# Kernel optimization log

Measured on AMD Instinct MI355X. Metric: run time of the kernel, lower is better.

Reference implementation:

```python
import jax, jax.numpy as jnp
import numpy as np

N = 50000   # nodes
E = 800000  # edges
IN, HID, OUT = 128, 128, 64


def setup_inputs() -> dict:
    key = jax.random.key(0)
    ks = jax.random.split(key, 16)
    x = jax.random.normal(ks[0], (N, IN), dtype=jnp.float32)
    src = jax.random.randint(ks[1], (E,), 0, N, dtype=jnp.int32)
    dst = jax.random.randint(ks[2], (E,), 0, N, dtype=jnp.int32)
    s = 1.0 / np.sqrt(IN)
    W_self1 = jax.random.normal(ks[3], (IN, HID), dtype=jnp.float32) * s
    W_neigh1 = jax.random.normal(ks[4], (IN, HID), dtype=jnp.float32) * s
    b1 = jnp.zeros((HID,), dtype=jnp.float32)
    W_self2 = jax.random.normal(ks[5], (HID, HID), dtype=jnp.float32) * s
    W_neigh2 = jax.random.normal(ks[6], (HID, HID), dtype=jnp.float32) * s
    b2 = jnp.zeros((HID,), dtype=jnp.float32)
    W_self3 = jax.random.normal(ks[7], (HID, OUT), dtype=jnp.float32) * s
    W_neigh3 = jax.random.normal(ks[8], (HID, OUT), dtype=jnp.float32) * s
    b3 = jnp.zeros((OUT,), dtype=jnp.float32)
    # dropout(p=0.5) masks, pre-scaled by 1/(1-p)
    keep = 0.5
    mask1 = (jax.random.uniform(ks[9], (N, HID)) < keep).astype(jnp.float32) / keep
    mask2 = (jax.random.uniform(ks[10], (N, HID)) < keep).astype(jnp.float32) / keep
    return dict(x=x, src=src, dst=dst,
                W_self1=W_self1, W_neigh1=W_neigh1, b1=b1,
                W_self2=W_self2, W_neigh2=W_neigh2, b2=b2,
                W_self3=W_self3, W_neigh3=W_neigh3, b3=b3,
                mask1=mask1, mask2=mask2)


def _mean_agg(h, src, dst):
    # gather source features, segment-sum into destinations, divide by in-degree
    summed = jax.ops.segment_sum(h[src], dst, num_segments=N)  # [N, d]
    deg = jax.ops.segment_sum(jnp.ones((E,), dtype=h.dtype), dst, num_segments=N)
    return summed / jnp.maximum(deg, 1.0)[:, None]


def _sage_layer(h, src, dst, W_self, W_neigh, b):
    h_neigh = _mean_agg(h, src, dst)
    return h @ W_self + h_neigh @ W_neigh + b


def reference(x, src, dst, W_self1, W_neigh1, b1, W_self2, W_neigh2, b2,
              W_self3, W_neigh3, b3, mask1, mask2):
    h = _sage_layer(x, src, dst, W_self1, W_neigh1, b1)
    h = jax.nn.relu(h) * mask1
    h = _sage_layer(h, src, dst, W_self2, W_neigh2, b2)
    h = jax.nn.relu(h) * mask2
    h = _sage_layer(h, src, dst, W_self3, W_neigh3, b3)
    return h
```

## Files before the change

### kernel.cpp

```cpp
#include <hip/hip_runtime.h>
#include <hip/hip_bf16.h>

#define DIN  128
#define DHID 128
#define DOUT 64

typedef short short8 __attribute__((ext_vector_type(8)));
typedef float f32x4  __attribute__((ext_vector_type(4)));

__device__ __forceinline__ ushort f2bf(float f) {
    union { float f; uint u; } c; c.f = f;
    uint u = c.u;
    return (ushort)((u + 0x7fff + ((u >> 16) & 1)) >> 16);
}
__device__ __forceinline__ float bf2f(uint h16) {
    union { uint u; float f; } c; c.u = h16 << 16;
    return c.f;
}
__device__ __forceinline__ float sb8(uint u, int k) {
    return (float)((int)(u << (24 - 8 * k)) >> 24);
}

__device__ __forceinline__ void wprep_dev(const float* __restrict__ W,
                                          ushort* __restrict__ Wt, int OUT, int idx) {
    int nn = idx >> 7;
    int k  = idx & 127;
    Wt[idx] = f2bf(W[(size_t)k * OUT + nn]);
}

__global__ __launch_bounds__(256)
void prep_all(const float* __restrict__ x, ushort* __restrict__ xb, int n4, int cvtB,
              const float* __restrict__ Ws1, const float* __restrict__ Wn1,
              const float* __restrict__ Ws2, const float* __restrict__ Wn2,
              const float* __restrict__ Ws3, const float* __restrict__ Wn3,
              ushort* __restrict__ Wst1, ushort* __restrict__ Wnt1,
              ushort* __restrict__ Wst2, ushort* __restrict__ Wnt2,
              ushort* __restrict__ Wst3, ushort* __restrict__ Wnt3) {
    int b = blockIdx.x;
    if (b < cvtB) {
        int i = b * 256 + threadIdx.x;
        if (i < n4) {
            float4 v = ((const float4*)x)[i];
            ushort4 o;
            o.x = f2bf(v.x); o.y = f2bf(v.y); o.z = f2bf(v.z); o.w = f2bf(v.w);
            ((ushort4*)xb)[i] = o;
        }
        return;
    }
    b -= cvtB;
    if (b < 64)  { wprep_dev(Ws1, Wst1, 128, b * 256 + threadIdx.x); return; }
    b -= 64;
    if (b < 64)  { wprep_dev(Wn1, Wnt1, 128, b * 256 + threadIdx.x); return; }
    b -= 64;
    if (b < 64)  { wprep_dev(Ws2, Wst2, 128, b * 256 + threadIdx.x); return; }
    b -= 64;
    if (b < 64)  { wprep_dev(Wn2, Wnt2, 128, b * 256 + threadIdx.x); return; }
    b -= 64;
    if (b < 32)  { wprep_dev(Ws3, Wst3, 64, b * 256 + threadIdx.x); return; }
    b -= 32;
    wprep_dev(Wn3, Wnt3, 64, b * 256 + threadIdx.x);
}

#define EB 4096

__global__ __launch_bounds__(256)
void bucket_count(const int* __restrict__ dst, int E, int* __restrict__ bkt_cnt) {
    __shared__ int c[256];
    const int t = threadIdx.x;
    c[t] = 0;
    __syncthreads();
    const int base = blockIdx.x * EB;
    const int end = min(base + EB, E);
    for (int i = base + t; i < end; i += 256)
        atomicAdd(&c[dst[i] >> 8], 1);
    __syncthreads();
    int v = c[t];
    if (v) atomicAdd(&bkt_cnt[t], v);
}

__global__ __launch_bounds__(256)
void bucket_scan(const int* __restrict__ bkt_cnt, int nbkt,
                 int* __restrict__ bkt_base, int* __restrict__ bkt_cur) {
    __shared__ int s[256];
    const int t = threadIdx.x;
    int v = (t < nbkt) ? bkt_cnt[t] : 0;
    s[t] = v;
    __syncthreads();
    for (int o = 1; o < 256; o <<= 1) {
        int u = (t >= o) ? s[t - o] : 0;
        __syncthreads();
        s[t] += u;
        __syncthreads();
    }
    if (t < nbkt) { bkt_base[t] = s[t] - v; bkt_cur[t] = s[t] - v; }
}

__global__ __launch_bounds__(256)
void bucket_fill(const int* __restrict__ src, const int* __restrict__ dst, int E,
                 int* __restrict__ bkt_cur, uint2* __restrict__ pairs) {
    __shared__ int c[256];
    __shared__ int startl[256];
    __shared__ int ofs[256];
    const int t = threadIdx.x;
    c[t] = 0;
    __syncthreads();
    const int base = blockIdx.x * EB;
    const int end = min(base + EB, E);
    for (int i = base + t; i < end; i += 256)
        atomicAdd(&c[dst[i] >> 8], 1);
    __syncthreads();
    int v = c[t];
    startl[t] = v ? atomicAdd(&bkt_cur[t], v) : 0;
    ofs[t] = 0;
    __syncthreads();
    for (int i = base + t; i < end; i += 256) {
        int d = dst[i];
        int b = d >> 8;
        int p = startl[b] + atomicAdd(&ofs[b], 1);
        pairs[p] = make_uint2((uint)src[i], (uint)(d & 255));
    }
}

__global__ __launch_bounds__(256)
void bucket_csr(const uint2* __restrict__ pairs, const int* __restrict__ bkt_base,
                const int* __restrict__ bkt_cnt, int* __restrict__ row_ptr,
                int* __restrict__ esrc, int N, int E, int nbkt) {
    constexpr int CAP = 6144;
    __shared__ uint2 pl[CAP];
    __shared__ int cnt[256];
    __shared__ int rs[256];
    __shared__ int sc[256];
    const int bkt = blockIdx.x;
    const int t = threadIdx.x;
    const int ebase = bkt_base[bkt];
    const int ecnt  = bkt_cnt[bkt];
    cnt[t] = 0;
    __syncthreads();
    const bool fits = (ecnt <= CAP);
    if (fits) {
        for (int i = t; i < ecnt; i += 256) {
            uint2 p = pairs[ebase + i];
            pl[i] = p;
            atomicAdd(&cnt[p.y], 1);
        }
    } else {
        for (int i = t; i < ecnt; i += 256)
            atomicAdd(&cnt[pairs[ebase + i].y], 1);
    }
    __syncthreads();
    int own = cnt[t];
    sc[t] = own;
    __syncthreads();
    for (int o = 1; o < 256; o <<= 1) {
        int u = (t >= o) ? sc[t - o] : 0;
        __syncthreads();
        sc[t] += u;
        __syncthreads();
    }
    rs[t] = sc[t] - own;
    const int node = bkt * 256 + t;
    if (node < N) row_ptr[node] = ebase + rs[t];
    if (bkt == nbkt - 1 && t == 0) row_ptr[N] = E;
    __syncthreads();
    if (fits) {
        for (int i = t; i < ecnt; i += 256) {
            uint2 p = pl[i];
            int pos = atomicAdd(&rs[p.y], 1);
            esrc[ebase + pos] = (int)p.x;
        }
    } else {
        for (int i = t; i < ecnt; i += 256) {
            uint2 p = pairs[ebase + i];
            int pos = atomicAdd(&rs[p.y], 1);
            esrc[ebase + pos] = (int)p.x;
        }
    }
}

template<int OUTW>
__global__ __launch_bounds__(256)
void sage_gemm(const ushort* __restrict__ Hb,
               const ushort* __restrict__ Wst,
               const ushort* __restrict__ Wnt,
               ushort* __restrict__ S,
               signed char* __restrict__ Gq,
               float* __restrict__ Gsc,
               int n) {
    constexpr int NT = OUTW / 16;
    __shared__ ushort Wl[2][OUTW * 128];

    const int tid  = threadIdx.x;
    const int lane = tid & 63;
    const int wave = tid >> 6;
    const int rg   = wave >> 1;
    const int isG  = wave & 1;
    const int m16  = lane & 15;
    const int kb   = lane >> 4;
    const int rbase = blockIdx.x * 64 + rg * 32;

    {
        const uint4* s4 = (const uint4*)Wst;
        const uint4* n4 = (const uint4*)Wnt;
        uint4* ls = (uint4*)&Wl[0][0];
        uint4* ln = (uint4*)&Wl[1][0];
#pragma unroll
        for (int j = tid; j < OUTW * 128 / 8; j += 256) {
            ls[j] = s4[j];
            ln[j] = n4[j];
        }
    }

    short8 a[2][4];
#pragma unroll
    for (int mt = 0; mt < 2; ++mt) {
        int arow = rbase + mt * 16 + m16;
        if (arow >= n) arow = n - 1;
        const ushort* __restrict__ Ap = &Hb[(size_t)arow * 128 + kb * 8];
#pragma unroll
        for (int c = 0; c < 4; ++c)
            a[mt][c] = *(const short8*)(Ap + c * 32);
    }

    __syncthreads();

    f32x4 acc[2][NT];
#pragma unroll
    for (int mt = 0; mt < 2; ++mt)
#pragma unroll
        for (int t = 0; t < NT; ++t) acc[mt][t] = (f32x4)(0.f);

    const ushort* __restrict__ Wp = &Wl[isG][0];
#pragma unroll
    for (int t = 0; t < NT; ++t) {
#pragma unroll
        for (int c = 0; c < 4; ++c) {
            short8 b = *(const short8*)&Wp[(t * 16 + m16) * 128 + c * 32 + kb * 8];
            acc[0][t] = __builtin_amdgcn_mfma_f32_16x16x32_bf16(a[0][c], b, acc[0][t], 0, 0, 0);
            acc[1][t] = __builtin_amdgcn_mfma_f32_16x16x32_bf16(a[1][c], b, acc[1][t], 0, 0, 0);
        }
    }

#pragma unroll
    for (int mt = 0; mt < 2; ++mt) {
        const int rb = rbase + mt * 16;
        if (!isG) {
#pragma unroll
            for (int r = 0; r < 4; ++r) {
                int row = rb + kb * 4 + r;
                if (row >= n) continue;
#pragma unroll
                for (int t = 0; t < NT; ++t)
                    S[(size_t)row * OUTW + t * 16 + m16] = f2bf(acc[mt][t][r]);
            }
        } else {
#pragma unroll
            for (int r = 0; r < 4; ++r) {
                float mx = 0.f;
#pragma unroll
                for (int t = 0; t < NT; ++t) mx = fmaxf(mx, fabsf(acc[mt][t][r]));
                mx = fmaxf(mx, __shfl_xor(mx, 1));
                mx = fmaxf(mx, __shfl_xor(mx, 2));
                mx = fmaxf(mx, __shfl_xor(mx, 4));
                mx = fmaxf(mx, __shfl_xor(mx, 8));
                int row = rb + kb * 4 + r;
                if (row >= n) continue;
                float inv = (mx > 0.f) ? 127.f / mx : 0.f;
                if (m16 == 0) Gsc[row] = mx * (1.f / 127.f);
#pragma unroll
                for (int t = 0; t < NT; ++t) {
                    int q = (int)rintf(acc[mt][t][r] * inv);
                    q = max(-127, min(127, q));
                    Gq[(size_t)row * OUTW + t * 16 + m16] = (signed char)q;
                }
            }
        }
    }
}

__device__ __forceinline__ void acc8(float* af, uint2 v, float sc) {
    af[0] += sc * sb8(v.x, 0); af[1] += sc * sb8(v.x, 1);
    af[2] += sc * sb8(v.x, 2); af[3] += sc * sb8(v.x, 3);
    af[4] += sc * sb8(v.y, 0); af[5] += sc * sb8(v.y, 1);
    af[6] += sc * sb8(v.y, 2); af[7] += sc * sb8(v.y, 3);
}
__device__ __forceinline__ void acc4(float* af, uint v, float sc) {
    af[0] += sc * sb8(v, 0); af[1] += sc * sb8(v, 1);
    af[2] += sc * sb8(v, 2); af[3] += sc * sb8(v, 3);
}

template<int OUTW, bool FINAL>
__global__ __launch_bounds__(256)
void sage_gather(const signed char* __restrict__ Gq, const float* __restrict__ Gsc,
                 const ushort* __restrict__ S, const float* __restrict__ bias,
                 const float* __restrict__ mask,
                 const int* __restrict__ row_ptr, const int* __restrict__ esrc,
                 void* __restrict__ outv, int n) {
    const int lane = threadIdx.x & 63;
    const int wave = threadIdx.x >> 6;
    const int qw   = lane >> 4;
    const int l16  = lane & 15;

#pragma unroll
    for (int j = 0; j < 2; ++j) {
        const int node = blockIdx.x * 32 + (wave * 4 + qw) * 2 + j;
        if (node >= n) continue;
        const int s = row_ptr[node];
        const int e = row_ptr[node + 1];
        const float inv = 1.f / fmaxf((float)(e - s), 1.f);

        if (OUTW == 128) {
            const signed char* __restrict__ gp = Gq + l16 * 8;
            float af[8] = {0.f, 0.f, 0.f, 0.f, 0.f, 0.f, 0.f, 0.f};
            int i = s;
            for (; i + 3 < e; i += 4) {
                int n0 = esrc[i], n1 = esrc[i + 1], n2 = esrc[i + 2], n3 = esrc[i + 3];
                uint2 v0 = *(const uint2*)&gp[(size_t)n0 * 128];
                uint2 v1 = *(const uint2*)&gp[(size_t)n1 * 128];
                uint2 v2 = *(const uint2*)&gp[(size_t)n2 * 128];
                uint2 v3 = *(const uint2*)&gp[(size_t)n3 * 128];
                float c0 = Gsc[n0], c1 = Gsc[n1], c2 = Gsc[n2], c3 = Gsc[n3];
                acc8(af, v0, c0); acc8(af, v1, c1); acc8(af, v2, c2); acc8(af, v3, c3);
            }
            for (; i < e; ++i) {
                int ns = esrc[i];
                uint2 v = *(const uint2*)&gp[(size_t)ns * 128];
                acc8(af, v, Gsc[ns]);
            }
            const int col0 = l16 * 8;
            uint4 sv = *(const uint4*)&S[(size_t)node * 128 + col0];
            float4 b0 = *(const float4*)&bias[col0];
            float4 b1 = *(const float4*)&bias[col0 + 4];
            float z[8];
            z[0] = bf2f(sv.x & 0xffffu) + af[0] * inv + b0.x;
            z[1] = bf2f(sv.x >> 16)     + af[1] * inv + b0.y;
            z[2] = bf2f(sv.y & 0xffffu) + af[2] * inv + b0.z;
            z[3] = bf2f(sv.y >> 16)     + af[3] * inv + b0.w;
            z[4] = bf2f(sv.z & 0xffffu) + af[4] * inv + b1.x;
            z[5] = bf2f(sv.z >> 16)     + af[5] * inv + b1.y;
            z[6] = bf2f(sv.w & 0xffffu) + af[6] * inv + b1.z;
            z[7] = bf2f(sv.w >> 16)     + af[7] * inv + b1.w;
            float4 m0 = *(const float4*)&mask[(size_t)node * 128 + col0];
            float4 m1 = *(const float4*)&mask[(size_t)node * 128 + col0 + 4];
            z[0] = fmaxf(z[0], 0.f) * m0.x; z[1] = fmaxf(z[1], 0.f) * m0.y;
            z[2] = fmaxf(z[2], 0.f) * m0.z; z[3] = fmaxf(z[3], 0.f) * m0.w;
            z[4] = fmaxf(z[4], 0.f) * m1.x; z[5] = fmaxf(z[5], 0.f) * m1.y;
            z[6] = fmaxf(z[6], 0.f) * m1.z; z[7] = fmaxf(z[7], 0.f) * m1.w;
            uint4 pk;
            pk.x = (uint)f2bf(z[0]) | ((uint)f2bf(z[1]) << 16);
            pk.y = (uint)f2bf(z[2]) | ((uint)f2bf(z[3]) << 16);
            pk.z = (uint)f2bf(z[4]) | ((uint)f2bf(z[5]) << 16);
            pk.w = (uint)f2bf(z[6]) | ((uint)f2bf(z[7]) << 16);
            *(uint4*)&((ushort*)outv)[(size_t)node * 128 + col0] = pk;
        } else {
            const signed char* __restrict__ gp = Gq + l16 * 4;
            float af[4] = {0.f, 0.f, 0.f, 0.f};
            int i = s;
            for (; i + 3 < e; i += 4) {
                int n0 = esrc[i], n1 = esrc[i + 1], n2 = esrc[i + 2], n3 = esrc[i + 3];
                uint v0 = *(const uint*)&gp[(size_t)n0 * 64];
                uint v1 = *(const uint*)&gp[(size_t)n1 * 64];
                uint v2 = *(const uint*)&gp[(size_t)n2 * 64];
                uint v3 = *(const uint*)&gp[(size_t)n3 * 64];
                float c0 = Gsc[n0], c1 = Gsc[n1], c2 = Gsc[n2], c3 = Gsc[n3];
                acc4(af, v0, c0); acc4(af, v1, c1); acc4(af, v2, c2); acc4(af, v3, c3);
            }
            for (; i < e; ++i) {
                int ns = esrc[i];
                uint v = *(const uint*)&gp[(size_t)ns * 64];
                acc4(af, v, Gsc[ns]);
            }
            const int col0 = l16 * 4;
            uint2 sv = *(const uint2*)&S[(size_t)node * 64 + col0];
            float4 b0 = *(const float4*)&bias[col0];
            float4 z;
            z.x = bf2f(sv.x & 0xffffu) + af[0] * inv + b0.x;
            z.y = bf2f(sv.x >> 16)     + af[1] * inv + b0.y;
            z.z = bf2f(sv.y & 0xffffu) + af[2] * inv + b0.z;
            z.w = bf2f(sv.y >> 16)     + af[3] * inv + b0.w;
            *(float4*)&((float*)outv)[(size_t)node * 64 + col0] = z;
        }
    }
}

extern "C" void kernel_launch(void* const* d_in, const int* in_sizes, int n_in,
                              void* d_out, int out_size, void* d_ws, size_t ws_size,
                              hipStream_t stream) {
    const float* x   = (const float*)d_in[0];
    const int*   src = (const int*)d_in[1];
    const int*   dst = (const int*)d_in[2];
    const float* Ws1 = (const float*)d_in[3];
    const float* Wn1 = (const float*)d_in[4];
    const float* b1  = (const float*)d_in[5];
    const float* Ws2 = (const float*)d_in[6];
    const float* Wn2 = (const float*)d_in[7];
    const float* b2  = (const float*)d_in[8];
    const float* Ws3 = (const float*)d_in[9];
    const float* Wn3 = (const float*)d_in[10];
    const float* b3  = (const float*)d_in[11];
    const float* mask1 = (const float*)d_in[12];
    const float* mask2 = (const float*)d_in[13];
    float* out = (float*)d_out;

    const int N = in_sizes[0] / DIN;
    const int E = in_sizes[1];
    const int nbkt = (N + 255) >> 8;

    char* ws = (char*)d_ws;
    int* bkt_cnt  = (int*)ws;
    int* bkt_base = bkt_cnt + 256;
    int* bkt_cur  = bkt_base + 256;
    int* row_ptr  = bkt_cur + 256;
    int* esrc     = row_ptr + (N + 1);
    size_t off = ((size_t)(768 + N + 1 + E) * sizeof(int) + 255) & ~(size_t)255;
    uint2* pairs = (uint2*)(ws + off);   off += (size_t)E * 8;
    ushort* xb   = (ushort*)(ws + off);  off += (size_t)N * 128 * 2;
    ushort* h1b  = (ushort*)(ws + off);  off += (size_t)N * 128 * 2;
    ushort* h2b  = (ushort*)(ws + off);  off += (size_t)N * 128 * 2;
    ushort* S    = (ushort*)(ws + off);  off += (size_t)N * 128 * 2;
    signed char* Gq = (signed char*)(ws + off); off += (size_t)N * 128;
    float* Gsc   = (float*)(ws + off);   off += (size_t)N * 4;
    ushort* Wst1 = (ushort*)(ws + off);  off += 128 * 128 * 2;
    ushort* Wnt1 = (ushort*)(ws + off);  off += 128 * 128 * 2;
    ushort* Wst2 = (ushort*)(ws + off);  off += 128 * 128 * 2;
    ushort* Wnt2 = (ushort*)(ws + off);  off += 128 * 128 * 2;
    ushort* Wst3 = (ushort*)(ws + off);  off += 64 * 128 * 2;
    ushort* Wnt3 = (ushort*)(ws + off);  off += 64 * 128 * 2;

    const int n4 = N * 128 / 4;
    const int cvtB = (n4 + 255) / 256;
    const int ebB = (E + EB - 1) / EB;

    hipMemsetAsync(bkt_cnt, 0, 256 * sizeof(int), stream);
    prep_all<<<cvtB + 4 * 64 + 2 * 32, 256, 0, stream>>>(
        x, xb, n4, cvtB,
        Ws1, Wn1, Ws2, Wn2, Ws3, Wn3,
        Wst1, Wnt1, Wst2, Wnt2, Wst3, Wnt3);

    bucket_count<<<ebB, 256, 0, stream>>>(dst, E, bkt_cnt);
    bucket_scan<<<1, 256, 0, stream>>>(bkt_cnt, nbkt, bkt_base, bkt_cur);
    bucket_fill<<<ebB, 256, 0, stream>>>(src, dst, E, bkt_cur, pairs);
    bucket_csr<<<nbkt, 256, 0, stream>>>(pairs, bkt_base, bkt_cnt, row_ptr, esrc, N, E, nbkt);

    const int gemmB = (N + 63) / 64;
    const int gathB = (N + 31) / 32;

    sage_gemm<128><<<gemmB, 256, 0, stream>>>(xb, Wst1, Wnt1, S, Gq, Gsc, N);
    sage_gather<128, false><<<gathB, 256, 0, stream>>>(Gq, Gsc, S, b1, mask1, row_ptr, esrc, h1b, N);
    sage_gemm<128><<<gemmB, 256, 0, stream>>>(h1b, Wst2, Wnt2, S, Gq, Gsc, N);
    sage_gather<128, false><<<gathB, 256, 0, stream>>>(Gq, Gsc, S, b2, mask2, row_ptr, esrc, h2b, N);
    sage_gemm<64><<<gemmB, 256, 0, stream>>>(h2b, Wst3, Wnt3, S, Gq, Gsc, N);
    sage_gather<64, true><<<gathB, 256, 0, stream>>>(Gq, Gsc, S, b3, nullptr, row_ptr, esrc, out, N);
}
```

Before: 304.4 us.

## Fuse bucket count into prep kernel and split CSR rows by source half

Folds the destination-bucket counting pass into the prep_all kernel, removing one launch. The CSR build now sorts each row's edges into two segments by whether the source index falls below or above N/2, and records a per-node mid pointer. The gather kernels walk the two segments separately, which appears aimed at improving cache locality of the random source-row reads. The cost is an extra N-int array, doubled shared-memory counters, and two shorter unrolled loops per node with more remainder iterations.

```diff
diff --git a/kernel.cpp b/kernel.cpp
--- a/kernel.cpp
+++ b/kernel.cpp
@@ -20,6 +20,8 @@
 __device__ __forceinline__ float sb8(uint u, int k) {
     return (float)((int)(u << (24 - 8 * k)) >> 24);
 }
+
+#define EB 4096
 
 __device__ __forceinline__ void wprep_dev(const float* __restrict__ W,
                                           ushort* __restrict__ Wt, int OUT, int idx) {
@@ -29,16 +31,32 @@
 }
 
 __global__ __launch_bounds__(256)
-void prep_all(const float* __restrict__ x, ushort* __restrict__ xb, int n4, int cvtB,
+void prep_all(const int* __restrict__ dst, int* __restrict__ bkt_cnt, int E, int countB,
+              const float* __restrict__ x, ushort* __restrict__ xb, int n4, int cvtB,
               const float* __restrict__ Ws1, const float* __restrict__ Wn1,
               const float* __restrict__ Ws2, const float* __restrict__ Wn2,
               const float* __restrict__ Ws3, const float* __restrict__ Wn3,
               ushort* __restrict__ Wst1, ushort* __restrict__ Wnt1,
               ushort* __restrict__ Wst2, ushort* __restrict__ Wnt2,
               ushort* __restrict__ Wst3, ushort* __restrict__ Wnt3) {
+    __shared__ int c[256];
     int b = blockIdx.x;
+    const int t = threadIdx.x;
+    if (b < countB) {
+        c[t] = 0;
+        __syncthreads();
+        const int base = b * EB;
+        const int end = min(base + EB, E);
+        for (int i = base + t; i < end; i += 256)
+            atomicAdd(&c[dst[i] >> 8], 1);
+        __syncthreads();
+        int v = c[t];
+        if (v) atomicAdd(&bkt_cnt[t], v);
+        return;
+    }
+    b -= countB;
     if (b < cvtB) {
-        int i = b * 256 + threadIdx.x;
+        int i = b * 256 + t;
         if (i < n4) {
             float4 v = ((const float4*)x)[i];
             ushort4 o;
@@ -48,34 +66,17 @@
         return;
     }
     b -= cvtB;
-    if (b < 64)  { wprep_dev(Ws1, Wst1, 128, b * 256 + threadIdx.x); return; }
+    if (b < 64)  { wprep_dev(Ws1, Wst1, 128, b * 256 + t); return; }
     b -= 64;
-    if (b < 64)  { wprep_dev(Wn1, Wnt1, 128, b * 256 + threadIdx.x); return; }
+    if (b < 64)  { wprep_dev(Wn1, Wnt1, 128, b * 256 + t); return; }
     b -= 64;
-    if (b < 64)  { wprep_dev(Ws2, Wst2, 128, b * 256 + threadIdx.x); return; }
+    if (b < 64)  { wprep_dev(Ws2, Wst2, 128, b * 256 + t); return; }
     b -= 64;
-    if (b < 64)  { wprep_dev(Wn2, Wnt2, 128, b * 256 + threadIdx.x); return; }
+    if (b < 64)  { wprep_dev(Wn2, Wnt2, 128, b * 256 + t); return; }
     b -= 64;
-    if (b < 32)  { wprep_dev(Ws3, Wst3, 64, b * 256 + threadIdx.x); return; }
+    if (b < 32)  { wprep_dev(Ws3, Wst3, 64, b * 256 + t); return; }
     b -= 32;
-    wprep_dev(Wn3, Wnt3, 64, b * 256 + threadIdx.x);
-}
-
-#define EB 4096
-
-__global__ __launch_bounds__(256)
-void bucket_count(const int* __restrict__ dst, int E, int* __restrict__ bkt_cnt) {
-    __shared__ int c[256];
-    const int t = threadIdx.x;
-    c[t] = 0;
-    __syncthreads();
-    const int base = blockIdx.x * EB;
-    const int end = min(base + EB, E);
-    for (int i = base + t; i < end; i += 256)
-        atomicAdd(&c[dst[i] >> 8], 1);
-    __syncthreads();
-    int v = c[t];
-    if (v) atomicAdd(&bkt_cnt[t], v);
+    wprep_dev(Wn3, Wnt3, 64, b * 256 + t);
 }
 
 __global__ __launch_bounds__(256)
@@ -124,32 +125,37 @@
 __global__ __launch_bounds__(256)
 void bucket_csr(const uint2* __restrict__ pairs, const int* __restrict__ bkt_base,
                 const int* __restrict__ bkt_cnt, int* __restrict__ row_ptr,
-                int* __restrict__ esrc, int N, int E, int nbkt) {
+                int* __restrict__ mid_ptr, int* __restrict__ esrc,
+                int N, int E, int nbkt, int half) {
     constexpr int CAP = 6144;
     __shared__ uint2 pl[CAP];
-    __shared__ int cnt[256];
-    __shared__ int rs[256];
+    __shared__ int cnt[512];
+    __shared__ int rs[512];
     __shared__ int sc[256];
     const int bkt = blockIdx.x;
     const int t = threadIdx.x;
     const int ebase = bkt_base[bkt];
     const int ecnt  = bkt_cnt[bkt];
-    cnt[t] = 0;
+    cnt[t] = 0; cnt[t + 256] = 0;
     __syncthreads();
     const bool fits = (ecnt <= CAP);
     if (fits) {
         for (int i = t; i < ecnt; i += 256) {
             uint2 p = pairs[ebase + i];
             pl[i] = p;
-            atomicAdd(&cnt[p.y], 1);
+            atomicAdd(&cnt[p.y * 2 + (p.x >= (uint)half)], 1);
         }
     } else {
-        for (int i = t; i < ecnt; i += 256)
-            atomicAdd(&cnt[pairs[ebase + i].y], 1);
-    }
-    __syncthreads();
-    int own = cnt[t];
-    sc[t] = own;
+        for (int i = t; i < ecnt; i += 256) {
+            uint2 p = pairs[ebase + i];
+            atomicAdd(&cnt[p.y * 2 + (p.x >= (uint)half)], 1);
+        }
+    }
+    __syncthreads();
+    int c0 = cnt[2 * t];
+    int c1 = cnt[2 * t + 1];
+    int pr = c0 + c1;
+    sc[t] = pr;
     __syncthreads();
     for (int o = 1; o < 256; o <<= 1) {
         int u = (t >= o) ? sc[t - o] : 0;
@@ -157,21 +163,26 @@
         sc[t] += u;
         __syncthreads();
     }
-    rs[t] = sc[t] - own;
+    int excl = sc[t] - pr;
+    rs[2 * t] = excl;
+    rs[2 * t + 1] = excl + c0;
     const int node = bkt * 256 + t;
-    if (node < N) row_ptr[node] = ebase + rs[t];
+    if (node < N) {
+        row_ptr[node] = ebase + excl;
+        mid_ptr[node] = ebase + excl + c0;
+    }
     if (bkt == nbkt - 1 && t == 0) row_ptr[N] = E;
     __syncthreads();
     if (fits) {
         for (int i = t; i < ecnt; i += 256) {
             uint2 p = pl[i];
-            int pos = atomicAdd(&rs[p.y], 1);
+            int pos = atomicAdd(&rs[p.y * 2 + (p.x >= (uint)half)], 1);
             esrc[ebase + pos] = (int)p.x;
         }
     } else {
         for (int i = t; i < ecnt; i += 256) {
             uint2 p = pairs[ebase + i];
-            int pos = atomicAdd(&rs[p.y], 1);
+            int pos = atomicAdd(&rs[p.y * 2 + (p.x >= (uint)half)], 1);
             esrc[ebase + pos] = (int)p.x;
         }
     }
@@ -288,12 +299,54 @@
     af[2] += sc * sb8(v, 2); af[3] += sc * sb8(v, 3);
 }
 
+__device__ __forceinline__ void gath_seg128(const signed char* __restrict__ gp,
+                                            const int* __restrict__ esrc,
+                                            const float* __restrict__ Gsc,
+                                            int s, int e, float* af) {
+    int i = s;
+    for (; i + 3 < e; i += 4) {
+        int n0 = esrc[i], n1 = esrc[i + 1], n2 = esrc[i + 2], n3 = esrc[i + 3];
+        uint2 v0 = *(const uint2*)&gp[(size_t)n0 * 128];
+        uint2 v1 = *(const uint2*)&gp[(size_t)n1 * 128];
+        uint2 v2 = *(const uint2*)&gp[(size_t)n2 * 128];
+        uint2 v3 = *(const uint2*)&gp[(size_t)n3 * 128];
+        float c0 = Gsc[n0], c1 = Gsc[n1], c2 = Gsc[n2], c3 = Gsc[n3];
+        acc8(af, v0, c0); acc8(af, v1, c1); acc8(af, v2, c2); acc8(af, v3, c3);
+    }
+    for (; i < e; ++i) {
+        int ns = esrc[i];
+        uint2 v = *(const uint2*)&gp[(size_t)ns * 128];
+        acc8(af, v, Gsc[ns]);
+    }
+}
+__device__ __forceinline__ void gath_seg64(const signed char* __restrict__ gp,
+                                           const int* __restrict__ esrc,
+                                           const float* __restrict__ Gsc,
+                                           int s, int e, float* af) {
+    int i = s;
+    for (; i + 3 < e; i += 4) {
+        int n0 = esrc[i], n1 = esrc[i + 1], n2 = esrc[i + 2], n3 = esrc[i + 3];
+        uint v0 = *(const uint*)&gp[(size_t)n0 * 64];
+        uint v1 = *(const uint*)&gp[(size_t)n1 * 64];
+        uint v2 = *(const uint*)&gp[(size_t)n2 * 64];
+        uint v3 = *(const uint*)&gp[(size_t)n3 * 64];
+        float c0 = Gsc[n0], c1 = Gsc[n1], c2 = Gsc[n2], c3 = Gsc[n3];
+        acc4(af, v0, c0); acc4(af, v1, c1); acc4(af, v2, c2); acc4(af, v3, c3);
+    }
+    for (; i < e; ++i) {
+        int ns = esrc[i];
+        uint v = *(const uint*)&gp[(size_t)ns * 64];
+        acc4(af, v, Gsc[ns]);
+    }
+}
+
 template<int OUTW, bool FINAL>
 __global__ __launch_bounds__(256)
 void sage_gather(const signed char* __restrict__ Gq, const float* __restrict__ Gsc,
                  const ushort* __restrict__ S, const float* __restrict__ bias,
                  const float* __restrict__ mask,
-                 const int* __restrict__ row_ptr, const int* __restrict__ esrc,
+                 const int* __restrict__ row_ptr, const int* __restrict__ mid_ptr,
+                 const int* __restrict__ esrc,
                  void* __restrict__ outv, int n) {
     const int lane = threadIdx.x & 63;
     const int wave = threadIdx.x >> 6;
@@ -305,27 +358,15 @@
         const int node = blockIdx.x * 32 + (wave * 4 + qw) * 2 + j;
         if (node >= n) continue;
         const int s = row_ptr[node];
+        const int m = mid_ptr[node];
         const int e = row_ptr[node + 1];
         const float inv = 1.f / fmaxf((float)(e - s), 1.f);
 
         if (OUTW == 128) {
             const signed char* __restrict__ gp = Gq + l16 * 8;
             float af[8] = {0.f, 0.f, 0.f, 0.f, 0.f, 0.f, 0.f, 0.f};
-            int i = s;
-            for (; i + 3 < e; i += 4) {
-                int n0 = esrc[i], n1 = esrc[i + 1], n2 = esrc[i + 2], n3 = esrc[i + 3];
-                uint2 v0 = *(const uint2*)&gp[(size_t)n0 * 128];
-                uint2 v1 = *(const uint2*)&gp[(size_t)n1 * 128];
-                uint2 v2 = *(const uint2*)&gp[(size_t)n2 * 128];
-                uint2 v3 = *(const uint2*)&gp[(size_t)n3 * 128];
-                float c0 = Gsc[n0], c1 = Gsc[n1], c2 = Gsc[n2], c3 = Gsc[n3];
-                acc8(af, v0, c0); acc8(af, v1, c1); acc8(af, v2, c2); acc8(af, v3, c3);
-            }
-            for (; i < e; ++i) {
-                int ns = esrc[i];
-                uint2 v = *(const uint2*)&gp[(size_t)ns * 128];
-                acc8(af, v, Gsc[ns]);
-            }
+            gath_seg128(gp, esrc, Gsc, s, m, af);
+            gath_seg128(gp, esrc, Gsc, m, e, af);
             const int col0 = l16 * 8;
             uint4 sv = *(const uint4*)&S[(size_t)node * 128 + col0];
             float4 b0 = *(const float4*)&bias[col0];
@@ -354,21 +395,8 @@
         } else {
             const signed char* __restrict__ gp = Gq + l16 * 4;
             float af[4] = {0.f, 0.f, 0.f, 0.f};
-            int i = s;
-            for (; i + 3 < e; i += 4) {
-                int n0 = esrc[i], n1 = esrc[i + 1], n2 = esrc[i + 2], n3 = esrc[i + 3];
-                uint v0 = *(const uint*)&gp[(size_t)n0 * 64];
-                uint v1 = *(const uint*)&gp[(size_t)n1 * 64];
-                uint v2 = *(const uint*)&gp[(size_t)n2 * 64];
-                uint v3 = *(const uint*)&gp[(size_t)n3 * 64];
-                float c0 = Gsc[n0], c1 = Gsc[n1], c2 = Gsc[n2], c3 = Gsc[n3];
-                acc4(af, v0, c0); acc4(af, v1, c1); acc4(af, v2, c2); acc4(af, v3, c3);
-            }
-            for (; i < e; ++i) {
-                int ns = esrc[i];
-                uint v = *(const uint*)&gp[(size_t)ns * 64];
-                acc4(af, v, Gsc[ns]);
-            }
+            gath_seg64(gp, esrc, Gsc, s, m, af);
+            gath_seg64(gp, esrc, Gsc, m, e, af);
             const int col0 = l16 * 4;
             uint2 sv = *(const uint2*)&S[(size_t)node * 64 + col0];
             float4 b0 = *(const float4*)&bias[col0];
@@ -404,14 +432,16 @@
     const int N = in_sizes[0] / DIN;
     const int E = in_sizes[1];
     const int nbkt = (N + 255) >> 8;
+    const int half = N >> 1;
 
     char* ws = (char*)d_ws;
     int* bkt_cnt  = (int*)ws;
     int* bkt_base = bkt_cnt + 256;
     int* bkt_cur  = bkt_base + 256;
     int* row_ptr  = bkt_cur + 256;
-    int* esrc     = row_ptr + (N + 1);
-    size_t off = ((size_t)(768 + N + 1 + E) * sizeof(int) + 255) & ~(size_t)255;
+    int* mid_ptr  = row_ptr + (N + 1);
+    int* esrc     = mid_ptr + N;
+    size_t off = ((size_t)(768 + 2 * N + 1 + E) * sizeof(int) + 255) & ~(size_t)255;
     uint2* pairs = (uint2*)(ws + off);   off += (size_t)E * 8;
     ushort* xb   = (ushort*)(ws + off);  off += (size_t)N * 128 * 2;
     ushort* h1b  = (ushort*)(ws + off);  off += (size_t)N * 128 * 2;
@@ -431,23 +461,24 @@
     const int ebB = (E + EB - 1) / EB;
 
     hipMemsetAsync(bkt_cnt, 0, 256 * sizeof(int), stream);
-    prep_all<<<cvtB + 4 * 64 + 2 * 32, 256, 0, stream>>>(
+    prep_all<<<ebB + cvtB + 4 * 64 + 2 * 32, 256, 0, stream>>>(
+        dst, bkt_cnt, E, ebB,
         x, xb, n4, cvtB,
         Ws1, Wn1, Ws2, Wn2, Ws3, Wn3,
         Wst1, Wnt1, Wst2, Wnt2, Wst3, Wnt3);
 
-    bucket_count<<<ebB, 256, 0, stream>>>(dst, E, bkt_cnt);
     bucket_scan<<<1, 256, 0, stream>>>(bkt_cnt, nbkt, bkt_base, bkt_cur);
     bucket_fill<<<ebB, 256, 0, stream>>>(src, dst, E, bkt_cur, pairs);
-    bucket_csr<<<nbkt, 256, 0, stream>>>(pairs, bkt_base, bkt_cnt, row_ptr, esrc, N, E, nbkt);
+    bucket_csr<<<nbkt, 256, 0, stream>>>(pairs, bkt_base, bkt_cnt, row_ptr, mid_ptr,
+                                         esrc, N, E, nbkt, half);
 
     const int gemmB = (N + 63) / 64;
     const int gathB = (N + 31) / 32;
 
     sage_gemm<128><<<gemmB, 256, 0, stream>>>(xb, Wst1, Wnt1, S, Gq, Gsc, N);
-    sage_gather<128, false><<<gathB, 256, 0, stream>>>(Gq, Gsc, S, b1, mask1, row_ptr, esrc, h1b, N);
+    sage_gather<128, false><<<gathB, 256, 0, stream>>>(Gq, Gsc, S, b1, mask1, row_ptr, mid_ptr, esrc, h1b, N);
     sage_gemm<128><<<gemmB, 256, 0, stream>>>(h1b, Wst2, Wnt2, S, Gq, Gsc, N);
-    sage_gather<128, false><<<gathB, 256, 0, stream>>>(Gq, Gsc, S, b2, mask2, row_ptr, esrc, h2b, N);
+    sage_gather<128, false><<<gathB, 256, 0, stream>>>(Gq, Gsc, S, b2, mask2, row_ptr, mid_ptr, esrc, h2b, N);
     sage_gemm<64><<<gemmB, 256, 0, stream>>>(h2b, Wst3, Wnt3, S, Gq, Gsc, N);
-    sage_gather<64, true><<<gathB, 256, 0, stream>>>(Gq, Gsc, S, b3, nullptr, row_ptr, esrc, out, N);
-}
+    sage_gather<64, true><<<gathB, 256, 0, stream>>>(Gq, Gsc, S, b3, nullptr, row_ptr, mid_ptr, esrc, out, N);
+}
```

Measured after the change: 297.8 us. 2.2% less time.

## Split int8 gather tables into 64-column planes and pack CSR pairs

Applied to the files above, without the earlier changes.

The 128-wide quantized neighbour table is stored as two 64-byte-per-row planes, and each 128-wide gather runs as two passes, one per plane, so each pass's random-access working set is halved and may stay cache-resident. The bucket-count pass is folded into the prep kernel to remove a launch. Edge pairs are packed into one 32-bit word (src<<8 | local dst), which halves pair traffic and lets the CSR bucket buffer hold twice as many entries. The trade-off is two gather launches per layer that each re-read esrc, row_ptr and Gsc, and the packing assumes src fits in 24 bits.

```diff
diff --git a/kernel.cpp b/kernel.cpp
--- a/kernel.cpp
+++ b/kernel.cpp
@@ -20,6 +20,8 @@
 __device__ __forceinline__ float sb8(uint u, int k) {
     return (float)((int)(u << (24 - 8 * k)) >> 24);
 }
+
+#define EB 4096
 
 __device__ __forceinline__ void wprep_dev(const float* __restrict__ W,
                                           ushort* __restrict__ Wt, int OUT, int idx) {
@@ -29,16 +31,32 @@
 }
 
 __global__ __launch_bounds__(256)
-void prep_all(const float* __restrict__ x, ushort* __restrict__ xb, int n4, int cvtB,
+void prep_all(const int* __restrict__ dst, int* __restrict__ bkt_cnt, int E, int countB,
+              const float* __restrict__ x, ushort* __restrict__ xb, int n4, int cvtB,
               const float* __restrict__ Ws1, const float* __restrict__ Wn1,
               const float* __restrict__ Ws2, const float* __restrict__ Wn2,
               const float* __restrict__ Ws3, const float* __restrict__ Wn3,
               ushort* __restrict__ Wst1, ushort* __restrict__ Wnt1,
               ushort* __restrict__ Wst2, ushort* __restrict__ Wnt2,
               ushort* __restrict__ Wst3, ushort* __restrict__ Wnt3) {
+    __shared__ int c[256];
     int b = blockIdx.x;
+    const int t = threadIdx.x;
+    if (b < countB) {
+        c[t] = 0;
+        __syncthreads();
+        const int base = b * EB;
+        const int end = min(base + EB, E);
+        for (int i = base + t; i < end; i += 256)
+            atomicAdd(&c[dst[i] >> 8], 1);
+        __syncthreads();
+        int v = c[t];
+        if (v) atomicAdd(&bkt_cnt[t], v);
+        return;
+    }
+    b -= countB;
     if (b < cvtB) {
-        int i = b * 256 + threadIdx.x;
+        int i = b * 256 + t;
         if (i < n4) {
             float4 v = ((const float4*)x)[i];
             ushort4 o;
@@ -48,34 +66,17 @@
         return;
     }
     b -= cvtB;
-    if (b < 64)  { wprep_dev(Ws1, Wst1, 128, b * 256 + threadIdx.x); return; }
+    if (b < 64)  { wprep_dev(Ws1, Wst1, 128, b * 256 + t); return; }
     b -= 64;
-    if (b < 64)  { wprep_dev(Wn1, Wnt1, 128, b * 256 + threadIdx.x); return; }
+    if (b < 64)  { wprep_dev(Wn1, Wnt1, 128, b * 256 + t); return; }
     b -= 64;
-    if (b < 64)  { wprep_dev(Ws2, Wst2, 128, b * 256 + threadIdx.x); return; }
+    if (b < 64)  { wprep_dev(Ws2, Wst2, 128, b * 256 + t); return; }
     b -= 64;
-    if (b < 64)  { wprep_dev(Wn2, Wnt2, 128, b * 256 + threadIdx.x); return; }
+    if (b < 64)  { wprep_dev(Wn2, Wnt2, 128, b * 256 + t); return; }
     b -= 64;
-    if (b < 32)  { wprep_dev(Ws3, Wst3, 64, b * 256 + threadIdx.x); return; }
+    if (b < 32)  { wprep_dev(Ws3, Wst3, 64, b * 256 + t); return; }
     b -= 32;
-    wprep_dev(Wn3, Wnt3, 64, b * 256 + threadIdx.x);
-}
-
-#define EB 4096
-
-__global__ __launch_bounds__(256)
-void bucket_count(const int* __restrict__ dst, int E, int* __restrict__ bkt_cnt) {
-    __shared__ int c[256];
-    const int t = threadIdx.x;
-    c[t] = 0;
-    __syncthreads();
-    const int base = blockIdx.x * EB;
-    const int end = min(base + EB, E);
-    for (int i = base + t; i < end; i += 256)
-        atomicAdd(&c[dst[i] >> 8], 1);
-    __syncthreads();
-    int v = c[t];
-    if (v) atomicAdd(&bkt_cnt[t], v);
+    wprep_dev(Wn3, Wnt3, 64, b * 256 + t);
 }
 
 __global__ __launch_bounds__(256)
@@ -97,7 +98,7 @@
 
 __global__ __launch_bounds__(256)
 void bucket_fill(const int* __restrict__ src, const int* __restrict__ dst, int E,
-                 int* __restrict__ bkt_cur, uint2* __restrict__ pairs) {
+                 int* __restrict__ bkt_cur, uint* __restrict__ pairs) {
     __shared__ int c[256];
     __shared__ int startl[256];
     __shared__ int ofs[256];
@@ -117,16 +118,16 @@
         int d = dst[i];
         int b = d >> 8;
         int p = startl[b] + atomicAdd(&ofs[b], 1);
-        pairs[p] = make_uint2((uint)src[i], (uint)(d & 255));
-    }
-}
-
-__global__ __launch_bounds__(256)
-void bucket_csr(const uint2* __restrict__ pairs, const int* __restrict__ bkt_base,
+        pairs[p] = ((uint)src[i] << 8) | (uint)(d & 255);
+    }
+}
+
+__global__ __launch_bounds__(256)
+void bucket_csr(const uint* __restrict__ pairs, const int* __restrict__ bkt_base,
                 const int* __restrict__ bkt_cnt, int* __restrict__ row_ptr,
                 int* __restrict__ esrc, int N, int E, int nbkt) {
-    constexpr int CAP = 6144;
-    __shared__ uint2 pl[CAP];
+    constexpr int CAP = 12288;
+    __shared__ uint pl[CAP];
     __shared__ int cnt[256];
     __shared__ int rs[256];
     __shared__ int sc[256];
@@ -139,13 +140,13 @@
     const bool fits = (ecnt <= CAP);
     if (fits) {
         for (int i = t; i < ecnt; i += 256) {
-            uint2 p = pairs[ebase + i];
+            uint p = pairs[ebase + i];
             pl[i] = p;
-            atomicAdd(&cnt[p.y], 1);
+            atomicAdd(&cnt[p & 255u], 1);
         }
     } else {
         for (int i = t; i < ecnt; i += 256)
-            atomicAdd(&cnt[pairs[ebase + i].y], 1);
+            atomicAdd(&cnt[pairs[ebase + i] & 255u], 1);
     }
     __syncthreads();
     int own = cnt[t];
@@ -164,15 +165,15 @@
     __syncthreads();
     if (fits) {
         for (int i = t; i < ecnt; i += 256) {
-            uint2 p = pl[i];
-            int pos = atomicAdd(&rs[p.y], 1);
-            esrc[ebase + pos] = (int)p.x;
+            uint p = pl[i];
+            int pos = atomicAdd(&rs[p & 255u], 1);
+            esrc[ebase + pos] = (int)(p >> 8);
         }
     } else {
         for (int i = t; i < ecnt; i += 256) {
-            uint2 p = pairs[ebase + i];
-            int pos = atomicAdd(&rs[p.y], 1);
-            esrc[ebase + pos] = (int)p.x;
+            uint p = pairs[ebase + i];
+            int pos = atomicAdd(&rs[p & 255u], 1);
+            esrc[ebase + pos] = (int)(p >> 8);
         }
     }
 }
@@ -183,7 +184,8 @@
                const ushort* __restrict__ Wst,
                const ushort* __restrict__ Wnt,
                ushort* __restrict__ S,
-               signed char* __restrict__ Gq,
+               signed char* __restrict__ Gq0,
+               signed char* __restrict__ Gq1,
                float* __restrict__ Gsc,
                int n) {
     constexpr int NT = OUTW / 16;
@@ -270,35 +272,33 @@
                 for (int t = 0; t < NT; ++t) {
                     int q = (int)rintf(acc[mt][t][r] * inv);
                     q = max(-127, min(127, q));
-                    Gq[(size_t)row * OUTW + t * 16 + m16] = (signed char)q;
+                    signed char* gq = (OUTW == 128 && t >= 4) ? Gq1 : Gq0;
+                    gq[(size_t)row * 64 + (t & 3) * 16 + m16] = (signed char)q;
                 }
             }
         }
     }
 }
 
-__device__ __forceinline__ void acc8(float* af, uint2 v, float sc) {
-    af[0] += sc * sb8(v.x, 0); af[1] += sc * sb8(v.x, 1);
-    af[2] += sc * sb8(v.x, 2); af[3] += sc * sb8(v.x, 3);
-    af[4] += sc * sb8(v.y, 0); af[5] += sc * sb8(v.y, 1);
-    af[6] += sc * sb8(v.y, 2); af[7] += sc * sb8(v.y, 3);
-}
 __device__ __forceinline__ void acc4(float* af, uint v, float sc) {
     af[0] += sc * sb8(v, 0); af[1] += sc * sb8(v, 1);
     af[2] += sc * sb8(v, 2); af[3] += sc * sb8(v, 3);
 }
 
-template<int OUTW, bool FINAL>
-__global__ __launch_bounds__(256)
-void sage_gather(const signed char* __restrict__ Gq, const float* __restrict__ Gsc,
-                 const ushort* __restrict__ S, const float* __restrict__ bias,
-                 const float* __restrict__ mask,
-                 const int* __restrict__ row_ptr, const int* __restrict__ esrc,
-                 void* __restrict__ outv, int n) {
+template<int HW>
+__global__ __launch_bounds__(256)
+void sage_gather_half(const signed char* __restrict__ Gqp,
+                      const float* __restrict__ Gsc,
+                      const ushort* __restrict__ S,
+                      const float* __restrict__ bias, const float* __restrict__ mask,
+                      const int* __restrict__ row_ptr, const int* __restrict__ esrc,
+                      ushort* __restrict__ hout,
+                      int plane, int n) {
     const int lane = threadIdx.x & 63;
     const int wave = threadIdx.x >> 6;
     const int qw   = lane >> 4;
     const int l16  = lane & 15;
+    const signed char* __restrict__ gp = Gqp + l16 * 4;
 
 #pragma unroll
     for (int j = 0; j < 2; ++j) {
@@ -308,77 +308,89 @@
         const int e = row_ptr[node + 1];
         const float inv = 1.f / fmaxf((float)(e - s), 1.f);
 
-        if (OUTW == 128) {
-            const signed char* __restrict__ gp = Gq + l16 * 8;
-            float af[8] = {0.f, 0.f, 0.f, 0.f, 0.f, 0.f, 0.f, 0.f};
-            int i = s;
-            for (; i + 3 < e; i += 4) {
-                int n0 = esrc[i], n1 = esrc[i + 1], n2 = esrc[i + 2], n3 = esrc[i + 3];
-                uint2 v0 = *(const uint2*)&gp[(size_t)n0 * 128];
-                uint2 v1 = *(const uint2*)&gp[(size_t)n1 * 128];
-                uint2 v2 = *(const uint2*)&gp[(size_t)n2 * 128];
-                uint2 v3 = *(const uint2*)&gp[(size_t)n3 * 128];
-                float c0 = Gsc[n0], c1 = Gsc[n1], c2 = Gsc[n2], c3 = Gsc[n3];
-                acc8(af, v0, c0); acc8(af, v1, c1); acc8(af, v2, c2); acc8(af, v3, c3);
+        float af[4] = {0.f, 0.f, 0.f, 0.f};
+        int i = s;
+        for (; i + 7 < e; i += 8) {
+            uint v[8]; float c[8];
+#pragma unroll
+            for (int k = 0; k < 8; ++k) {
+                int ns = esrc[i + k];
+                v[k] = *(const uint*)&gp[(size_t)ns * 64];
+                c[k] = Gsc[ns];
             }
-            for (; i < e; ++i) {
-                int ns = esrc[i];
-                uint2 v = *(const uint2*)&gp[(size_t)ns * 128];
-                acc8(af, v, Gsc[ns]);
+#pragma unroll
+            for (int k = 0; k < 8; ++k) acc4(af, v[k], c[k]);
+        }
+        for (; i < e; ++i) {
+            int ns = esrc[i];
+            uint v = *(const uint*)&gp[(size_t)ns * 64];
+            acc4(af, v, Gsc[ns]);
+        }
+
+        const int col0 = plane * 64 + l16 * 4;
+        uint2 sv = *(const uint2*)&S[(size_t)node * HW + col0];
+        float4 b0 = *(const float4*)&bias[col0];
+        float4 m0 = *(const float4*)&mask[(size_t)node * HW + col0];
+        float z0 = bf2f(sv.x & 0xffffu) + af[0] * inv + b0.x;
+        float z1 = bf2f(sv.x >> 16)     + af[1] * inv + b0.y;
+        float z2 = bf2f(sv.y & 0xffffu) + af[2] * inv + b0.z;
+        float z3 = bf2f(sv.y >> 16)     + af[3] * inv + b0.w;
+        z0 = fmaxf(z0, 0.f) * m0.x; z1 = fmaxf(z1, 0.f) * m0.y;
+        z2 = fmaxf(z2, 0.f) * m0.z; z3 = fmaxf(z3, 0.f) * m0.w;
+        uint2 pk;
+        pk.x = (uint)f2bf(z0) | ((uint)f2bf(z1) << 16);
+        pk.y = (uint)f2bf(z2) | ((uint)f2bf(z3) << 16);
+        *(uint2*)&hout[(size_t)node * HW + col0] = pk;
+    }
+}
+
+__global__ __launch_bounds__(256)
+void sage_gather_final(const signed char* __restrict__ Gq0, const float* __restrict__ Gsc,
+                       const ushort* __restrict__ S, const float* __restrict__ bias,
+                       const int* __restrict__ row_ptr, const int* __restrict__ esrc,
+                       float* __restrict__ out, int n) {
+    const int lane = threadIdx.x & 63;
+    const int wave = threadIdx.x >> 6;
+    const int qw   = lane >> 4;
+    const int l16  = lane & 15;
+    const signed char* __restrict__ gp = Gq0 + l16 * 4;
+
+#pragma unroll
+    for (int j = 0; j < 2; ++j) {
+        const int node = blockIdx.x * 32 + (wave * 4 + qw) * 2 + j;
+        if (node >= n) continue;
+        const int s = row_ptr[node];
+        const int e = row_ptr[node + 1];
+        const float inv = 1.f / fmaxf((float)(e - s), 1.f);
+
+        float af[4] = {0.f, 0.f, 0.f, 0.f};
+        int i = s;
+        for (; i + 7 < e; i += 8) {
+            uint v[8]; float c[8];
+#pragma unroll
+            for (int k = 0; k < 8; ++k) {
+                int ns = esrc[i + k];
+                v[k] = *(const uint*)&gp[(size_t)ns * 64];
+                c[k] = Gsc[ns];
             }
-            const int col0 = l16 * 8;
-            uint4 sv = *(const uint4*)&S[(size_t)node * 128 + col0];
-            float4 b0 = *(const float4*)&bias[col0];
-            float4 b1 = *(const float4*)&bias[col0 + 4];
-            float z[8];
-            z[0] = bf2f(sv.x & 0xffffu) + af[0] * inv + b0.x;
-            z[1] = bf2f(sv.x >> 16)     + af[1] * inv + b0.y;
-            z[2] = bf2f(sv.y & 0xffffu) + af[2] * inv + b0.z;
-            z[3] = bf2f(sv.y >> 16)     + af[3] * inv + b0.w;
-            z[4] = bf2f(sv.z & 0xffffu) + af[4] * inv + b1.x;
-            z[5] = bf2f(sv.z >> 16)     + af[5] * inv + b1.y;
-            z[6] = bf2f(sv.w & 0xffffu) + af[6] * inv + b1.z;
-            z[7] = bf2f(sv.w >> 16)     + af[7] * inv + b1.w;
-            float4 m0 = *(const float4*)&mask[(size_t)node * 128 + col0];
-            float4 m1 = *(const float4*)&mask[(size_t)node * 128 + col0 + 4];
-            z[0] = fmaxf(z[0], 0.f) * m0.x; z[1] = fmaxf(z[1], 0.f) * m0.y;
-            z[2] = fmaxf(z[2], 0.f) * m0.z; z[3] = fmaxf(z[3], 0.f) * m0.w;
-            z[4] = fmaxf(z[4], 0.f) * m1.x; z[5] = fmaxf(z[5], 0.f) * m1.y;
-            z[6] = fmaxf(z[6], 0.f) * m1.z; z[7] = fmaxf(z[7], 0.f) * m1.w;
-            uint4 pk;
-            pk.x = (uint)f2bf(z[0]) | ((uint)f2bf(z[1]) << 16);
-            pk.y = (uint)f2bf(z[2]) | ((uint)f2bf(z[3]) << 16);
-            pk.z = (uint)f2bf(z[4]) | ((uint)f2bf(z[5]) << 16);
-            pk.w = (uint)f2bf(z[6]) | ((uint)f2bf(z[7]) << 16);
-            *(uint4*)&((ushort*)outv)[(size_t)node * 128 + col0] = pk;
-        } else {
-            const signed char* __restrict__ gp = Gq + l16 * 4;
-            float af[4] = {0.f, 0.f, 0.f, 0.f};
-            int i = s;
-            for (; i + 3 < e; i += 4) {
-                int n0 = esrc[i], n1 = esrc[i + 1], n2 = esrc[i + 2], n3 = esrc[i + 3];
-                uint v0 = *(const uint*)&gp[(size_t)n0 * 64];
-                uint v1 = *(const uint*)&gp[(size_t)n1 * 64];
-                uint v2 = *(const uint*)&gp[(size_t)n2 * 64];
-                uint v3 = *(const uint*)&gp[(size_t)n3 * 64];
-                float c0 = Gsc[n0], c1 = Gsc[n1], c2 = Gsc[n2], c3 = Gsc[n3];
-                acc4(af, v0, c0); acc4(af, v1, c1); acc4(af, v2, c2); acc4(af, v3, c3);
-            }
-            for (; i < e; ++i) {
-                int ns = esrc[i];
-                uint v = *(const uint*)&gp[(size_t)ns * 64];
-                acc4(af, v, Gsc[ns]);
-            }
-            const int col0 = l16 * 4;
-            uint2 sv = *(const uint2*)&S[(size_t)node * 64 + col0];
-            float4 b0 = *(const float4*)&bias[col0];
-            float4 z;
-            z.x = bf2f(sv.x & 0xffffu) + af[0] * inv + b0.x;
-            z.y = bf2f(sv.x >> 16)     + af[1] * inv + b0.y;
-            z.z = bf2f(sv.y & 0xffffu) + af[2] * inv + b0.z;
-            z.w = bf2f(sv.y >> 16)     + af[3] * inv + b0.w;
-            *(float4*)&((float*)outv)[(size_t)node * 64 + col0] = z;
-        }
+#pragma unroll
+            for (int k = 0; k < 8; ++k) acc4(af, v[k], c[k]);
+        }
+        for (; i < e; ++i) {
+            int ns = esrc[i];
+            uint v = *(const uint*)&gp[(size_t)ns * 64];
+            acc4(af, v, Gsc[ns]);
+        }
+
+        const int col0 = l16 * 4;
+        uint2 sv = *(const uint2*)&S[(size_t)node * 64 + col0];
+        float4 b0 = *(const float4*)&bias[col0];
+        float4 z;
+        z.x = bf2f(sv.x & 0xffffu) + af[0] * inv + b0.x;
+        z.y = bf2f(sv.x >> 16)     + af[1] * inv + b0.y;
+        z.z = bf2f(sv.y & 0xffffu) + af[2] * inv + b0.z;
+        z.w = bf2f(sv.y >> 16)     + af[3] * inv + b0.w;
+        *(float4*)&out[(size_t)node * 64 + col0] = z;
     }
 }
 
@@ -412,12 +424,13 @@
     int* row_ptr  = bkt_cur + 256;
     int* esrc     = row_ptr + (N + 1);
     size_t off = ((size_t)(768 + N + 1 + E) * sizeof(int) + 255) & ~(size_t)255;
-    uint2* pairs = (uint2*)(ws + off);   off += (size_t)E * 8;
+    uint* pairs  = (uint*)(ws + off);    off += (size_t)E * 4;
     ushort* xb   = (ushort*)(ws + off);  off += (size_t)N * 128 * 2;
     ushort* h1b  = (ushort*)(ws + off);  off += (size_t)N * 128 * 2;
     ushort* h2b  = (ushort*)(ws + off);  off += (size_t)N * 128 * 2;
     ushort* S    = (ushort*)(ws + off);  off += (size_t)N * 128 * 2;
-    signed char* Gq = (signed char*)(ws + off); off += (size_t)N * 128;
+    signed char* Gq0 = (signed char*)(ws + off); off += (size_t)N * 64;
+    signed char* Gq1 = (signed char*)(ws + off); off += (size_t)N * 64;
     float* Gsc   = (float*)(ws + off);   off += (size_t)N * 4;
     ushort* Wst1 = (ushort*)(ws + off);  off += 128 * 128 * 2;
     ushort* Wnt1 = (ushort*)(ws + off);  off += 128 * 128 * 2;
@@ -431,12 +444,12 @@
     const int ebB = (E + EB - 1) / EB;
 
     hipMemsetAsync(bkt_cnt, 0, 256 * sizeof(int), stream);
-    prep_all<<<cvtB + 4 * 64 + 2 * 32, 256, 0, stream>>>(
+    prep_all<<<ebB + cvtB + 4 * 64 + 2 * 32, 256, 0, stream>>>(
+        dst, bkt_cnt, E, ebB,
         x, xb, n4, cvtB,
         Ws1, Wn1, Ws2, Wn2, Ws3, Wn3,
         Wst1, Wnt1, Wst2, Wnt2, Wst3, Wnt3);
 
-    bucket_count<<<ebB, 256, 0, stream>>>(dst, E, bkt_cnt);
     bucket_scan<<<1, 256, 0, stream>>>(bkt_cnt, nbkt, bkt_base, bkt_cur);
     bucket_fill<<<ebB, 256, 0, stream>>>(src, dst, E, bkt_cur, pairs);
     bucket_csr<<<nbkt, 256, 0, stream>>>(pairs, bkt_base, bkt_cnt, row_ptr, esrc, N, E, nbkt);
@@ -444,10 +457,12 @@
     const int gemmB = (N + 63) / 64;
     const int gathB = (N + 31) / 32;
 
-    sage_gemm<128><<<gemmB, 256, 0, stream>>>(xb, Wst1, Wnt1, S, Gq, Gsc, N);
-    sage_gather<128, false><<<gathB, 256, 0, stream>>>(Gq, Gsc, S, b1, mask1, row_ptr, esrc, h1b, N);
-    sage_gemm<128><<<gemmB, 256, 0, stream>>>(h1b, Wst2, Wnt2, S, Gq, Gsc, N);
-    sage_gather<128, false><<<gathB, 256, 0, stream>>>(Gq, Gsc, S, b2, mask2, row_ptr, esrc, h2b, N);
-    sage_gemm<64><<<gemmB, 256, 0, stream>>>(h2b, Wst3, Wnt3, S, Gq, Gsc, N);
-    sage_gather<64, true><<<gathB, 256, 0, stream>>>(Gq, Gsc, S, b3, nullptr, row_ptr, esrc, out, N);
-}
+    sage_gemm<128><<<gemmB, 256, 0, stream>>>(xb, Wst1, Wnt1, S, Gq0, Gq1, Gsc, N);
+    sage_gather_half<128><<<gathB, 256, 0, stream>>>(Gq0, Gsc, S, b1, mask1, row_ptr, esrc, h1b, 0, N);
+    sage_gather_half<128><<<gathB, 256, 0, stream>>>(Gq1, Gsc, S, b1, mask1, row_ptr, esrc, h1b, 1, N);
+    sage_gemm<128><<<gemmB, 256, 0, stream>>>(h1b, Wst2, Wnt2, S, Gq0, Gq1, Gsc, N);
+    sage_gather_half<128><<<gathB, 256, 0, stream>>>(Gq0, Gsc, S, b2, mask2, row_ptr, esrc, h2b, 0, N);
+    sage_gather_half<128><<<gathB, 256, 0, stream>>>(Gq1, Gsc, S, b2, mask2, row_ptr, esrc, h2b, 1, N);
+    sage_gemm<64><<<gemmB, 256, 0, stream>>>(h2b, Wst3, Wnt3, S, Gq0, Gq1, Gsc, N);
+    sage_gather_final<<<gathB, 256, 0, stream>>>(Gq0, Gsc, S, b3, row_ptr, esrc, out, N);
+}
```

Result: slower. 339.4 us (+11.5%).
